# Optimization experiments

Measured on AMD Instinct MI355X. Metric: run time of the kernel, lower is better.

## Reference

```python
import jax, jax.numpy as jnp
import numpy as np

D_EEG = 256; D_QUERY = 256; D_MODEL = 256; NUM_HEADS = 8
D_HEAD = D_MODEL // NUM_HEADS; PROJ_DIM = 40
B = 32; N = 4096


def _rope(x):
    # x: (B, S, H, D) -- rotate along sequence dim with interleaved-pair convention
    S, D = x.shape[1], x.shape[-1]
    inv = 1.0 / (10000.0 ** (jnp.arange(0, D, 2, dtype=jnp.float32) / D))
    f = jnp.arange(S, dtype=jnp.float32)[:, None] * inv[None, :]        # (S, D/2)
    cos = jnp.repeat(jnp.cos(f), 2, axis=-1)[None, :, None, :]
    sin = jnp.repeat(jnp.sin(f), 2, axis=-1)[None, :, None, :]
    xp = x.reshape(x.shape[:-1] + (D // 2, 2))
    rot = jnp.stack([-xp[..., 1], xp[..., 0]], axis=-1).reshape(x.shape)
    return x * cos + rot * sin


def _ln(x, g, b):
    m = x.mean(-1, keepdims=True)
    v = x.var(-1, keepdims=True)
    return (x - m) / jnp.sqrt(v + 1e-5) * g + b


def _l2norm(x):
    return x / jnp.maximum(jnp.linalg.norm(x, axis=-1, keepdims=True), 1e-12)


def setup_inputs():
    key = jax.random.key(0)
    ks = jax.random.split(key, 16)

    def lin(k, din, dout):
        s = 1.0 / np.sqrt(din)
        w = jax.random.uniform(k, (din, dout), minval=-s, maxval=s, dtype=jnp.float32)
        b = jax.random.uniform(jax.random.fold_in(k, 1), (dout,), minval=-s, maxval=s, dtype=jnp.float32)
        return w, b

    eeg_w, eeg_b = lin(ks[0], D_EEG, D_MODEL)
    stim_w, stim_b = lin(ks[1], D_QUERY, D_MODEL)
    temp_w, temp_b = lin(ks[2], D_QUERY, D_MODEL)
    q_w, q_b = lin(ks[3], D_MODEL, D_MODEL)
    k_w, k_b = lin(ks[4], D_MODEL, D_MODEL)
    v_w, v_b = lin(ks[5], D_MODEL, D_MODEL)
    fc_w, fc_b = lin(ks[6], D_MODEL, PROJ_DIM)

    return {
        "eeg_feat": jax.random.normal(ks[7], (B, N, D_EEG), dtype=jnp.float32),
        "stim_feat": jax.random.normal(ks[8], (B, D_QUERY), dtype=jnp.float32),
        "temp_feat": jax.random.normal(ks[9], (B, D_QUERY), dtype=jnp.float32),
        "eeg_w": eeg_w, "eeg_b": eeg_b,
        "stim_w": stim_w, "stim_b": stim_b,
        "temp_w": temp_w, "temp_b": temp_b,
        "q_w": q_w, "q_b": q_b,
        "k_w": k_w, "k_b": k_b,
        "v_w": v_w, "v_b": v_b,
        "fc_w": fc_w, "fc_b": fc_b,
        "lnq_g": jnp.ones((D_MODEL,), jnp.float32), "lnq_b": jnp.zeros((D_MODEL,), jnp.float32),
        "lnk_g": jnp.ones((D_MODEL,), jnp.float32), "lnk_b": jnp.zeros((D_MODEL,), jnp.float32),
    }


def reference(eeg_feat, stim_feat, temp_feat, eeg_w, eeg_b, stim_w, stim_b,
              temp_w, temp_b, q_w, q_b, k_w, k_b, v_w, v_b, fc_w, fc_b,
              lnq_g, lnq_b, lnk_g, lnk_b):
    Bq = eeg_feat.shape[0]
    eeg = eeg_feat @ eeg_w + eeg_b                      # (B, N, D)
    stim = (stim_feat @ stim_w + stim_b)[:, None, :]
    temp = (temp_feat @ temp_w + temp_b)[:, None, :]
    query = jnp.concatenate([stim, temp], axis=1)        # (B, 2, D)

    query = _ln(query, lnq_g, lnq_b)
    kv = _ln(eeg, lnk_g, lnk_b)

    Q = (query @ q_w + q_b).reshape(Bq, 2, NUM_HEADS, D_HEAD)
    K = (kv @ k_w + k_b).reshape(Bq, -1, NUM_HEADS, D_HEAD)
    V = (kv @ v_w + v_b).reshape(Bq, -1, NUM_HEADS, D_HEAD)

    Q = _l2norm(_rope(Q))
    K = _l2norm(_rope(K))

    scores = jnp.einsum('bqhd,bkhd->bhqk', Q, K) / np.sqrt(D_HEAD)
    scale = jax.lax.stop_gradient(
        jnp.maximum(jnp.std(scores, axis=-1, ddof=1, keepdims=True), 1e-3))
    scores = jnp.tanh(scores / (2.0 * scale)) * (5.0 * scale)

    w = jax.nn.softmax(scores, axis=-1)
    w = (w + 1e-4) / (w.sum(-1, keepdims=True) + 1e-8)

    attn_out = jnp.einsum('bhqk,bkhd->bqhd', w, V).reshape(Bq, 2, D_MODEL)
    pooled = attn_out.mean(axis=1)
    logits = pooled @ fc_w + fc_b
    return logits, pooled, attn_out, query
```

## Files before the change

### kernel.cpp

```cpp
#include <hip/hip_runtime.h>
#include <hip/hip_bf16.h>
#include <math.h>

#define TID ((int)threadIdx.x)

typedef float f32x4 __attribute__((ext_vector_type(4)));
typedef short s16x8 __attribute__((ext_vector_type(8)));

__device__ __forceinline__ unsigned short f2bf(float f) {
  union { float f; unsigned u; } v; v.f = f;
  unsigned r = v.u + 0x7FFFu + ((v.u >> 16) & 1u);
  return (unsigned short)(r >> 16);
}
__device__ __forceinline__ float bf2f(unsigned short h) {
  union { unsigned u; float f; } v; v.u = ((unsigned)h) << 16;
  return v.f;
}

__global__ __launch_bounds__(256) void prep1_kernel(
    const float* __restrict__ We, const float* __restrict__ Wk,
    const float* __restrict__ g, const float* __restrict__ be,
    const float* __restrict__ bln, const float* __restrict__ kb,
    unsigned short* __restrict__ wf, float2* __restrict__ trig,
    float* __restrict__ ckv, float* __restrict__ gkv, float* __restrict__ bkv) {
  int blk = blockIdx.x;
  if (blk < 32) {
    int fi = blk * 256 + TID;
    int l = fi & 63, ks = (fi >> 6) & 7, cbG = fi >> 9;
    int col = cbG * 16 + (l & 15);
    int kbase = ks * 32 + ((l >> 4) & 3) * 8;
    s16x8 pk;
#pragma unroll
    for (int e = 0; e < 8; ++e) pk[e] = (short)f2bf(We[(size_t)(kbase + e) * 256 + col]);
    *(s16x8*)&wf[(size_t)fi * 8] = pk;
  } else if (blk < 288) {
    int e = (blk - 32) * 256 + TID;
    int n = e >> 4, p = e & 15;
    float inv = exp2f(-(float)p * 0.8304820237218406f);
    float a = (float)n * inv;
    trig[e] = make_float2(cosf(a), sinf(a));
  } else {
    int j = TID;
    float a1 = 0.f, a2 = 0.f, a3 = 0.f;
    for (int k = 0; k < 256; ++k) {
      float wkj = Wk[k * 256 + j];
      float gk = g[k];
      a1 = fmaf(be[k] * gk, wkj, a1);
      a2 = fmaf(gk, wkj, a2);
      a3 = fmaf(bln[k], wkj, a3);
    }
    ckv[j] = a1; gkv[j] = a2; bkv[j] = a3 + kb[j];
  }
}

__global__ __launch_bounds__(256) void prep2_kernel(
    const float* __restrict__ We, const float* __restrict__ Wk,
    const float* __restrict__ g, unsigned short* __restrict__ wf) {
  int j = blockIdx.x;
  __shared__ float a[256];
  __shared__ float WeC[256 * 33];
  a[TID] = g[TID] * Wk[TID * 256 + j];
  float acc = 0.f;
  for (int k0 = 0; k0 < 256; k0 += 32) {
    __syncthreads();
    const float4* src = (const float4*)&We[TID * 256 + k0];
#pragma unroll
    for (int q4 = 0; q4 < 8; ++q4) {
      float4 v = src[q4];
      WeC[TID * 33 + q4 * 4 + 0] = v.x;
      WeC[TID * 33 + q4 * 4 + 1] = v.y;
      WeC[TID * 33 + q4 * 4 + 2] = v.z;
      WeC[TID * 33 + q4 * 4 + 3] = v.w;
    }
    __syncthreads();
#pragma unroll
    for (int kk = 0; kk < 32; ++kk)
      acc = fmaf(WeC[TID * 33 + kk], a[k0 + kk], acc);
  }
  int cbG = 16 + (j >> 4), c = j & 15;
  int ks = TID >> 5, g3 = (TID >> 3) & 3, e = TID & 7;
  size_t pos = (((size_t)(cbG * 8 + ks) * 64) + g3 * 16 + c) * 8 + e;
  wf[pos] = f2bf(acc);
}

__global__ __launch_bounds__(256) void q_kernel(
    const float* __restrict__ stim_feat, const float* __restrict__ temp_feat,
    const float* __restrict__ stim_w, const float* __restrict__ stim_b,
    const float* __restrict__ temp_w, const float* __restrict__ temp_b,
    const float* __restrict__ q_w, const float* __restrict__ q_b,
    const float* __restrict__ lnq_g, const float* __restrict__ lnq_b,
    float* __restrict__ out_query, float* __restrict__ qhat) {
  int b = blockIdx.x >> 1, q = blockIdx.x & 1;
  __shared__ float f[256];
  __shared__ float red[8];
  const float* feat = (q ? temp_feat : stim_feat) + b * 256;
  const float* W = q ? temp_w : stim_w;
  const float* bias = q ? temp_b : stim_b;
  f[TID] = feat[TID];
  __syncthreads();
  float acc = bias[TID];
#pragma unroll 8
  for (int i = 0; i < 256; ++i) acc = fmaf(f[i], W[i * 256 + TID], acc);
  float s1 = acc, s2 = acc * acc;
#pragma unroll
  for (int m = 1; m < 64; m <<= 1) { s1 += __shfl_xor(s1, m, 64); s2 += __shfl_xor(s2, m, 64); }
  if ((TID & 63) == 0) { red[TID >> 6] = s1; red[4 + (TID >> 6)] = s2; }
  __syncthreads();
  s1 = red[0] + red[1] + red[2] + red[3];
  s2 = red[4] + red[5] + red[6] + red[7];
  float mean = s1 * (1.f / 256.f);
  float var = s2 * (1.f / 256.f) - mean * mean;
  float rstd = rsqrtf(var + 1e-5f);
  float qln = (acc - mean) * rstd * lnq_g[TID] + lnq_b[TID];
  out_query[(b * 2 + q) * 256 + TID] = qln;
  __syncthreads();
  f[TID] = qln;
  __syncthreads();
  float a2 = q_b[TID];
#pragma unroll 8
  for (int i = 0; i < 256; ++i) a2 = fmaf(f[i], q_w[i * 256 + TID], a2);
  __syncthreads();
  f[TID] = a2;
  __syncthreads();
  float partner = f[TID ^ 1];
  int p = (TID >> 1) & 15;
  float inv = exp2f(-(float)p * 0.8304820237218406f);
  float ang = (float)q * inv;
  float cc_ = cosf(ang), ss_ = sinf(ang);
  float r = (TID & 1) ? fmaf(a2, cc_, partner * ss_) : fmaf(a2, cc_, -partner * ss_);
  float sq = r * r;
#pragma unroll
  for (int m = 1; m < 32; m <<= 1) sq += __shfl_xor(sq, m, 32);
  float rs = 1.f / fmaxf(sqrtf(sq), 1e-12f);
  qhat[(b * 2 + q) * 256 + TID] = r * rs;
}

__global__ __launch_bounds__(256) void main2_kernel(
    const float* __restrict__ x,
    const float* __restrict__ eeg_b,
    const unsigned short* __restrict__ wf,
    const float2* __restrict__ trig,
    const float* __restrict__ qhat,
    const float* __restrict__ ckv,
    const float* __restrict__ gkv,
    const float* __restrict__ bkv,
    float2* __restrict__ stats,
    float* __restrict__ scores) {

  __shared__ __align__(16) unsigned short A[32 * 256];
  __shared__ float CV0[256];
  __shared__ float CV1[256];
  __shared__ float CV2[256];
  __shared__ float QH[512];
  __shared__ float PS[32 * 9];
  __shared__ float2 ST[32];

  const int tid = TID;
  const int w = tid >> 6, l = tid & 63, g = l >> 4, c = l & 15;
  const int r0 = blockIdx.x * 32;
  const int b = r0 >> 12;
  const int n0 = r0 & 4095;

#pragma unroll
  for (int i = 0; i < 4; ++i) {
    int ch = i * 256 + tid;
    int row = ch >> 5, cc = ch & 31;
    const float4* gp = (const float4*)(x + (size_t)(r0 + row) * 256 + cc * 8);
    float4 u0 = gp[0], u1 = gp[1];
    s16x8 pk;
    pk[0] = (short)f2bf(u0.x); pk[1] = (short)f2bf(u0.y);
    pk[2] = (short)f2bf(u0.z); pk[3] = (short)f2bf(u0.w);
    pk[4] = (short)f2bf(u1.x); pk[5] = (short)f2bf(u1.y);
    pk[6] = (short)f2bf(u1.z); pk[7] = (short)f2bf(u1.w);
    *(s16x8*)&A[row * 256 + ((cc ^ (row & 7)) * 8)] = pk;
  }
  CV0[tid] = ckv[tid]; CV1[tid] = gkv[tid]; CV2[tid] = bkv[tid];
  QH[tid] = qhat[(size_t)b * 512 + tid];
  QH[256 + tid] = qhat[(size_t)b * 512 + 256 + tid];
  __syncthreads();

  f32x4 acc[2][8];
#pragma unroll
  for (int rb = 0; rb < 2; ++rb)
#pragma unroll
    for (int cb = 0; cb < 8; ++cb) acc[rb][cb] = (f32x4){0.f, 0.f, 0.f, 0.f};
#pragma unroll
  for (int ks = 0; ks < 8; ++ks) {
    s16x8 af[2];
#pragma unroll
    for (int rb = 0; rb < 2; ++rb) {
      int row = rb * 16 + c; int kc = ks * 4 + g;
      af[rb] = *(const s16x8*)&A[row * 256 + ((kc ^ (row & 7)) * 8)];
    }
#pragma unroll
    for (int hb = 0; hb < 2; ++hb) {
      s16x8 bf4[4];
#pragma unroll
      for (int q4 = 0; q4 < 4; ++q4) {
        int cbG = w * 8 + hb * 4 + q4;
        bf4[q4] = *(const s16x8*)&wf[(size_t)((cbG * 8 + ks) * 64 + l) * 8];
      }
#pragma unroll
      for (int rb = 0; rb < 2; ++rb)
#pragma unroll
        for (int q4 = 0; q4 < 4; ++q4)
          acc[rb][hb * 4 + q4] = __builtin_amdgcn_mfma_f32_16x16x32_bf16(
              af[rb], bf4[q4], acc[rb][hb * 4 + q4], 0, 0, 0);
    }
  }

  if (w < 2) {
    float ebias[8];
#pragma unroll
    for (int cb = 0; cb < 8; ++cb) ebias[cb] = eeg_b[w * 128 + cb * 16 + c];
    float ps[2][4], pq[2][4];
#pragma unroll
    for (int rb = 0; rb < 2; ++rb)
#pragma unroll
      for (int r = 0; r < 4; ++r) {
        float s = 0.f, q2 = 0.f;
#pragma unroll
        for (int cb = 0; cb < 8; ++cb) {
          float v = acc[rb][cb][r] + ebias[cb];
          s += v; q2 += v * v;
        }
        ps[rb][r] = s; pq[rb][r] = q2;
      }
#pragma unroll
    for (int m = 1; m < 16; m <<= 1)
#pragma unroll
      for (int rb = 0; rb < 2; ++rb)
#pragma unroll
        for (int r = 0; r < 4; ++r) {
          ps[rb][r] += __shfl_xor(ps[rb][r], m, 64);
          pq[rb][r] += __shfl_xor(pq[rb][r], m, 64);
        }
    float outS = 0.f, outQ = 0.f;
#pragma unroll
    for (int rb = 0; rb < 2; ++rb)
#pragma unroll
      for (int r = 0; r < 4; ++r)
        if (c == rb * 4 + r) { outS = ps[rb][r]; outQ = pq[rb][r]; }
    if (c < 8) {
      int row = (c >> 2) * 16 + g * 4 + (c & 3);
      PS[row * 9 + w * 2 + 0] = outS;
      PS[row * 9 + w * 2 + 1] = outQ;
    }
  }
  __syncthreads();

  if (tid < 32) {
    float s = PS[tid * 9 + 0] + PS[tid * 9 + 2];
    float q2 = PS[tid * 9 + 1] + PS[tid * 9 + 3];
    float mean = s * (1.f / 256.f);
    float var = q2 * (1.f / 256.f) - mean * mean;
    float rstd = rsqrtf(var + 1e-5f);
    ST[tid] = make_float2(mean, rstd);
    stats[(size_t)r0 + tid] = make_float2(mean, rstd);
  }
  if (w >= 2) {
#pragma unroll
    for (int rb = 0; rb < 2; ++rb)
#pragma unroll
      for (int r = 0; r < 4; ++r) {
        int row = rb * 16 + g * 4 + r;
#pragma unroll
        for (int cb = 0; cb < 8; ++cb) {
          int kcol = (w - 2) * 128 + cb * 16 + c;
          A[row * 256 + (kcol ^ ((row & 7) * 8))] = f2bf(acc[rb][cb][r]);
        }
      }
  }
  __syncthreads();

  {
    int h = tid >> 5, row = tid & 31;
    float2 st = ST[row];
    float is = st.y, mis = st.x * st.y;
    const float2* tgp = trig + (size_t)(n0 + row) * 16;
    float ssq = 0.f, d0 = 0.f, d1 = 0.f;
#pragma unroll
    for (int j = 0; j < 4; ++j) {
      int u = h * 4 + j;
      s16x8 kvv = *(const s16x8*)&A[row * 256 + ((u ^ (row & 7)) * 8)];
      float2 t0 = tgp[j * 4 + 0], t1 = tgp[j * 4 + 1], t2 = tgp[j * 4 + 2], t3 = tgp[j * 4 + 3];
      float2 tg4[4] = {t0, t1, t2, t3};
#pragma unroll
      for (int t = 0; t < 4; ++t) {
        int col = h * 32 + j * 8 + 2 * t;
        float base0 = fmaf(CV0[col], is, fmaf(-mis, CV1[col], CV2[col]));
        float base1 = fmaf(CV0[col + 1], is, fmaf(-mis, CV1[col + 1], CV2[col + 1]));
        float k0 = fmaf(bf2f((unsigned short)kvv[2 * t]), is, base0);
        float k1 = fmaf(bf2f((unsigned short)kvv[2 * t + 1]), is, base1);
        float2 cs = tg4[t];
        float rv0 = k0 * cs.x - k1 * cs.y;
        float rv1 = fmaf(k1, cs.x, k0 * cs.y);
        ssq = fmaf(rv0, rv0, fmaf(rv1, rv1, ssq));
        d0 = fmaf(rv0, QH[col], fmaf(rv1, QH[col + 1], d0));
        d1 = fmaf(rv0, QH[256 + col], fmaf(rv1, QH[256 + col + 1], d1));
      }
    }
    float isv = 0.17677669529663687f / fmaxf(sqrtf(ssq), 1e-12f);
    scores[(size_t)((b * 8 + h) * 2 + 0) * 4096 + n0 + row] = d0 * isv;
    scores[(size_t)((b * 8 + h) * 2 + 1) * 4096 + n0 + row] = d1 * isv;
  }
}

__global__ __launch_bounds__(256) void wgt_kernel(
    const float* __restrict__ scores, const float2* __restrict__ stats,
    float* __restrict__ wbuf, float2* __restrict__ sbuf) {
  int b = blockIdx.x >> 3, h = blockIdx.x & 7;
  const float* s0p = scores + (size_t)((b * 8 + h) * 2 + 0) * 4096;
  const float* s1p = scores + (size_t)((b * 8 + h) * 2 + 1) * 4096;
  float sa[16], sb[16];
  float a1 = 0.f, a2 = 0.f, b1 = 0.f, b2 = 0.f;
#pragma unroll
  for (int i = 0; i < 16; ++i) {
    int k = i * 256 + TID;
    sa[i] = s0p[k]; sb[i] = s1p[k];
    a1 += sa[i]; a2 += sa[i] * sa[i];
    b1 += sb[i]; b2 += sb[i] * sb[i];
  }
  __shared__ float red[16];
  int w = TID >> 6;
#pragma unroll
  for (int m = 1; m < 64; m <<= 1) {
    a1 += __shfl_xor(a1, m, 64); a2 += __shfl_xor(a2, m, 64);
    b1 += __shfl_xor(b1, m, 64); b2 += __shfl_xor(b2, m, 64);
  }
  if ((TID & 63) == 0) { red[w * 4] = a1; red[w * 4 + 1] = a2; red[w * 4 + 2] = b1; red[w * 4 + 3] = b2; }
  __syncthreads();
  a1 = red[0] + red[4] + red[8] + red[12];
  a2 = red[1] + red[5] + red[9] + red[13];
  b1 = red[2] + red[6] + red[10] + red[14];
  b2 = red[3] + red[7] + red[11] + red[15];
  float va = (a2 - a1 * a1 * (1.f / 4096.f)) * (1.f / 4095.f);
  float vb = (b2 - b1 * b1 * (1.f / 4096.f)) * (1.f / 4095.f);
  float sga = fmaxf(sqrtf(fmaxf(va, 0.f)), 1e-3f);
  float sgb = fmaxf(sqrtf(fmaxf(vb, 0.f)), 1e-3f);
  float ia = 0.5f / sga, ib = 0.5f / sgb;
  float fa = 5.f * sga, fb = 5.f * sgb;
  float ea = 0.f, eb = 0.f;
#pragma unroll
  for (int i = 0; i < 16; ++i) {
    sa[i] = __expf(tanhf(sa[i] * ia) * fa);
    sb[i] = __expf(tanhf(sb[i] * ib) * fb);
    ea += sa[i]; eb += sb[i];
  }
#pragma unroll
  for (int m = 1; m < 64; m <<= 1) { ea += __shfl_xor(ea, m, 64); eb += __shfl_xor(eb, m, 64); }
  __syncthreads();
  if ((TID & 63) == 0) { red[w * 2] = ea; red[w * 2 + 1] = eb; }
  __syncthreads();
  ea = red[0] + red[2] + red[4] + red[6];
  eb = red[1] + red[3] + red[5] + red[7];
  float iea = 1.f / ea, ieb = 1.f / eb;
  float* w0 = wbuf + ((size_t)(b * 16) + h * 2 + 0) * 4096;
  float* w1 = w0 + 4096;
  float s1a = 0.f, s2a = 0.f, s1b = 0.f, s2b = 0.f;
#pragma unroll
  for (int i = 0; i < 16; ++i) {
    int k = i * 256 + TID;
    float2 st = stats[(size_t)b * 4096 + k];
    float wa = fmaf(sa[i], iea, 1e-4f);
    float wb = fmaf(sb[i], ieb, 1e-4f);
    float wta = wa * st.y, wtb = wb * st.y;
    w0[k] = wta; w1[k] = wtb;
    s1a += wta; s2a = fmaf(wta, st.x, s2a);
    s1b += wtb; s2b = fmaf(wtb, st.x, s2b);
  }
#pragma unroll
  for (int m = 1; m < 64; m <<= 1) {
    s1a += __shfl_xor(s1a, m, 64); s2a += __shfl_xor(s2a, m, 64);
    s1b += __shfl_xor(s1b, m, 64); s2b += __shfl_xor(s2b, m, 64);
  }
  __syncthreads();
  if ((TID & 63) == 0) { red[w * 4] = s1a; red[w * 4 + 1] = s2a; red[w * 4 + 2] = s1b; red[w * 4 + 3] = s2b; }
  __syncthreads();
  if (TID == 0) {
    sbuf[((size_t)(b * 8 + h)) * 2 + 0] =
        make_float2(red[0] + red[4] + red[8] + red[12], red[1] + red[5] + red[9] + red[13]);
    sbuf[((size_t)(b * 8 + h)) * 2 + 1] =
        make_float2(red[2] + red[6] + red[10] + red[14], red[3] + red[7] + red[11] + red[15]);
  }
}

__global__ __launch_bounds__(256) void ysum_kernel(
    const float* __restrict__ x, const float* __restrict__ wbuf,
    float* __restrict__ ypart) {
  int b = blockIdx.x >> 5, slab = blockIdx.x & 31;
  int h = TID >> 5, cg = TID & 31;
  const float* xb = x + ((size_t)(b * 4096 + slab * 128)) * 256 + cg * 8;
  const float* w0 = wbuf + ((size_t)(b * 16) + h * 2 + 0) * 4096 + slab * 128;
  const float* w1 = w0 + 4096;
  float y0[8], y1[8];
#pragma unroll
  for (int t = 0; t < 8; ++t) { y0[t] = 0.f; y1[t] = 0.f; }
#pragma unroll 4
  for (int r = 0; r < 128; ++r) {
    const float4* fp = (const float4*)(xb + (size_t)r * 256);
    float4 va = fp[0], vb4 = fp[1];
    float wa = w0[r], wc = w1[r];
    y0[0] = fmaf(wa, va.x, y0[0]);  y1[0] = fmaf(wc, va.x, y1[0]);
    y0[1] = fmaf(wa, va.y, y0[1]);  y1[1] = fmaf(wc, va.y, y1[1]);
    y0[2] = fmaf(wa, va.z, y0[2]);  y1[2] = fmaf(wc, va.z, y1[2]);
    y0[3] = fmaf(wa, va.w, y0[3]);  y1[3] = fmaf(wc, va.w, y1[3]);
    y0[4] = fmaf(wa, vb4.x, y0[4]); y1[4] = fmaf(wc, vb4.x, y1[4]);
    y0[5] = fmaf(wa, vb4.y, y0[5]); y1[5] = fmaf(wc, vb4.y, y1[5]);
    y0[6] = fmaf(wa, vb4.z, y0[6]); y1[6] = fmaf(wc, vb4.z, y1[6]);
    y0[7] = fmaf(wa, vb4.w, y0[7]); y1[7] = fmaf(wc, vb4.w, y1[7]);
  }
  float* yp = ypart + (((size_t)(b * 32 + slab) * 16) + h * 2) * 256 + cg * 8;
  *(float4*)&yp[0] = (float4){y0[0], y0[1], y0[2], y0[3]};
  *(float4*)&yp[4] = (float4){y0[4], y0[5], y0[6], y0[7]};
  *(float4*)&yp[256] = (float4){y1[0], y1[1], y1[2], y1[3]};
  *(float4*)&yp[260] = (float4){y1[4], y1[5], y1[6], y1[7]};
}

__global__ __launch_bounds__(256) void yz_kernel(
    const float* __restrict__ ypart, const float2* __restrict__ sbuf,
    const float* __restrict__ We, const float* __restrict__ be,
    const float* __restrict__ g, const float* __restrict__ bln,
    float* __restrict__ zbuf) {
  int b = blockIdx.x >> 4, hq = blockIdx.x & 15;
  __shared__ float Y[256];
  float s = 0.f;
#pragma unroll 8
  for (int sl = 0; sl < 32; ++sl)
    s += ypart[(((size_t)(b * 32 + sl) * 16) + hq) * 256 + TID];
  Y[TID] = s;
  __syncthreads();
  float2 s12 = sbuf[(size_t)b * 16 + hq];
  int k = TID;
  float t = s12.x * be[k];
#pragma unroll 8
  for (int cc = 0; cc < 256; ++cc)
    t = fmaf(Y[cc], We[cc * 256 + k], t);
  zbuf[((size_t)(b * 16) + hq) * 256 + k] = (t - s12.y) * g[k] + 1.4096f * bln[k];
}

__global__ __launch_bounds__(256) void att_kernel(
    const float* __restrict__ zbuf, const float* __restrict__ v_w,
    const float* __restrict__ v_b, float* __restrict__ out_attn,
    float* __restrict__ out_pooled) {
  int b = blockIdx.x >> 3, h = blockIdx.x & 7;
  __shared__ float ZA[2][256];
  __shared__ float ATTs[2][32];
  {
    int q = TID >> 7, cc = TID & 127;
    const float* zp = zbuf + ((size_t)(b * 16) + h * 2 + q) * 256;
    ZA[q][cc] = zp[cc];
    ZA[q][128 + cc] = zp[128 + cc];
  }
  __syncthreads();
  int q = TID >> 7, dl = (TID >> 2) & 31, quarter = TID & 3;
  int dout = h * 32 + dl;
  float ps = 0.f;
#pragma unroll 8
  for (int i = 0; i < 64; ++i) {
    int cc = quarter * 64 + i;
    ps = fmaf(ZA[q][cc], v_w[cc * 256 + dout], ps);
  }
  ps += __shfl_xor(ps, 1, 64);
  ps += __shfl_xor(ps, 2, 64);
  if (quarter == 0) {
    float val = ps + 1.4096f * v_b[dout];
    out_attn[(b * 2 + q) * 256 + dout] = val;
    ATTs[q][dl] = val;
  }
  __syncthreads();
  if (TID < 32) {
    out_pooled[b * 256 + h * 32 + TID] = 0.5f * (ATTs[0][TID] + ATTs[1][TID]);
  }
}

__global__ __launch_bounds__(256) void logit_kernel(
    const float* __restrict__ out_pooled, const float* __restrict__ fc_w,
    const float* __restrict__ fc_b, float* __restrict__ out_logits) {
  int b = blockIdx.x;
  __shared__ float P[256];
  P[TID] = out_pooled[b * 256 + TID];
  __syncthreads();
  if (TID < 40) {
    float acc = fc_b[TID];
#pragma unroll 8
    for (int i = 0; i < 256; ++i) acc = fmaf(P[i], fc_w[i * 40 + TID], acc);
    out_logits[b * 40 + TID] = acc;
  }
}

extern "C" void kernel_launch(void* const* d_in, const int* in_sizes, int n_in,
                              void* d_out, int out_size, void* d_ws, size_t ws_size,
                              hipStream_t stream) {
  (void)in_sizes; (void)n_in; (void)out_size; (void)ws_size;
  const float* eeg_feat  = (const float*)d_in[0];
  const float* stim_feat = (const float*)d_in[1];
  const float* temp_feat = (const float*)d_in[2];
  const float* eeg_w = (const float*)d_in[3];
  const float* eeg_b = (const float*)d_in[4];
  const float* stim_w = (const float*)d_in[5];
  const float* stim_b = (const float*)d_in[6];
  const float* temp_w = (const float*)d_in[7];
  const float* temp_b = (const float*)d_in[8];
  const float* q_w = (const float*)d_in[9];
  const float* q_b = (const float*)d_in[10];
  const float* k_w = (const float*)d_in[11];
  const float* k_b = (const float*)d_in[12];
  const float* v_w = (const float*)d_in[13];
  const float* v_b = (const float*)d_in[14];
  const float* fc_w = (const float*)d_in[15];
  const float* fc_b = (const float*)d_in[16];
  const float* lnq_g = (const float*)d_in[17];
  const float* lnq_b = (const float*)d_in[18];
  const float* lnk_g = (const float*)d_in[19];
  const float* lnk_b = (const float*)d_in[20];

  char* ws = (char*)d_ws;
  unsigned short* wfr = (unsigned short*)(ws + 0);
  float2* trig        = (float2*)(ws + 262144);
  float* qhat         = (float*)(ws + 786432);
  float* ckv          = (float*)(ws + 851968);
  float* gkv          = (float*)(ws + 852992);
  float* bkv          = (float*)(ws + 854016);
  float2* sbuf        = (float2*)(ws + 855040);
  float2* stats       = (float2*)(ws + 1048576);
  float* scores       = (float*)(ws + 2097152);
  float* wbuf         = (float*)(ws + 10485760);
  float* ypart        = (float*)(ws + 18874368);
  float* zbuf         = (float*)(ws + 35651584);

  float* out = (float*)d_out;
  float* out_logits = out;
  float* out_pooled = out + 1280;
  float* out_attn   = out + 9472;
  float* out_query  = out + 25856;

  prep1_kernel<<<289, 256, 0, stream>>>(eeg_w, k_w, lnk_g, eeg_b, lnk_b, k_b,
                                        wfr, trig, ckv, gkv, bkv);
  prep2_kernel<<<256, 256, 0, stream>>>(eeg_w, k_w, lnk_g, wfr);
  q_kernel<<<64, 256, 0, stream>>>(stim_feat, temp_feat, stim_w, stim_b,
                                   temp_w, temp_b, q_w, q_b, lnq_g, lnq_b,
                                   out_query, qhat);
  main2_kernel<<<4096, 256, 0, stream>>>(eeg_feat, eeg_b, wfr, trig, qhat,
                                         ckv, gkv, bkv, stats, scores);
  wgt_kernel<<<256, 256, 0, stream>>>(scores, stats, wbuf, sbuf);
  ysum_kernel<<<1024, 256, 0, stream>>>(eeg_feat, wbuf, ypart);
  yz_kernel<<<512, 256, 0, stream>>>(ypart, sbuf, eeg_w, eeg_b, lnk_g, lnk_b, zbuf);
  att_kernel<<<256, 256, 0, stream>>>(zbuf, v_w, v_b, out_attn, out_pooled);
  logit_kernel<<<32, 256, 0, stream>>>(out_pooled, fc_w, fc_b, out_logits);
}
```

Before: 216.8 us.

## Process four row tiles per block with register-prefetched next tile

The main scoring kernel now has each block handle 128 rows as four 32-row tiles, launching 1024 blocks instead of 4096. While the current tile's MFMA and epilogue run, the next tile's fp32 input and RoPE trig values are prefetched into registers. Trig values are staged in shared memory rather than read per thread from global. This is meant to hide global load latency behind compute and amortise per-block setup (qhat, LN constants), at the cost of more registers, extra barriers and fewer blocks for occupancy.

```diff
diff --git a/kernel.cpp b/kernel.cpp
--- a/kernel.cpp
+++ b/kernel.cpp
@@ -154,155 +154,190 @@
   __shared__ float QH[512];
   __shared__ float PS[32 * 9];
   __shared__ float2 ST[32];
+  __shared__ float COS[32][17];
+  __shared__ float SIN[32][17];
 
   const int tid = TID;
   const int w = tid >> 6, l = tid & 63, g = l >> 4, c = l & 15;
-  const int r0 = blockIdx.x * 32;
-  const int b = r0 >> 12;
-  const int n0 = r0 & 4095;
-
-#pragma unroll
-  for (int i = 0; i < 4; ++i) {
-    int ch = i * 256 + tid;
-    int row = ch >> 5, cc = ch & 31;
-    const float4* gp = (const float4*)(x + (size_t)(r0 + row) * 256 + cc * 8);
-    float4 u0 = gp[0], u1 = gp[1];
-    s16x8 pk;
-    pk[0] = (short)f2bf(u0.x); pk[1] = (short)f2bf(u0.y);
-    pk[2] = (short)f2bf(u0.z); pk[3] = (short)f2bf(u0.w);
-    pk[4] = (short)f2bf(u1.x); pk[5] = (short)f2bf(u1.y);
-    pk[6] = (short)f2bf(u1.z); pk[7] = (short)f2bf(u1.w);
-    *(s16x8*)&A[row * 256 + ((cc ^ (row & 7)) * 8)] = pk;
-  }
+  const int chunk0 = blockIdx.x * 128;
+  const int b = chunk0 >> 12;
+  const int n0b = chunk0 & 4095;
+
   CV0[tid] = ckv[tid]; CV1[tid] = gkv[tid]; CV2[tid] = bkv[tid];
   QH[tid] = qhat[(size_t)b * 512 + tid];
   QH[256 + tid] = qhat[(size_t)b * 512 + 256 + tid];
-  __syncthreads();
-
-  f32x4 acc[2][8];
-#pragma unroll
-  for (int rb = 0; rb < 2; ++rb)
-#pragma unroll
-    for (int cb = 0; cb < 8; ++cb) acc[rb][cb] = (f32x4){0.f, 0.f, 0.f, 0.f};
-#pragma unroll
-  for (int ks = 0; ks < 8; ++ks) {
-    s16x8 af[2];
-#pragma unroll
-    for (int rb = 0; rb < 2; ++rb) {
-      int row = rb * 16 + c; int kc = ks * 4 + g;
-      af[rb] = *(const s16x8*)&A[row * 256 + ((kc ^ (row & 7)) * 8)];
-    }
-#pragma unroll
-    for (int hb = 0; hb < 2; ++hb) {
-      s16x8 bf4[4];
-#pragma unroll
-      for (int q4 = 0; q4 < 4; ++q4) {
-        int cbG = w * 8 + hb * 4 + q4;
-        bf4[q4] = *(const s16x8*)&wf[(size_t)((cbG * 8 + ks) * 64 + l) * 8];
+
+  float4 sxa[4], sxb[4];
+  float2 tf0, tf1;
+  {
+    const float* xt = x + (size_t)chunk0 * 256;
+#pragma unroll
+    for (int i = 0; i < 4; ++i) {
+      int ch = i * 256 + tid, row = ch >> 5, cc = ch & 31;
+      const float4* gp = (const float4*)(xt + row * 256 + cc * 8);
+      sxa[i] = gp[0]; sxb[i] = gp[1];
+    }
+    tf0 = trig[(size_t)(n0b + (tid >> 4)) * 16 + (tid & 15)];
+    tf1 = trig[(size_t)(n0b + 16 + (tid >> 4)) * 16 + (tid & 15)];
+  }
+
+  for (int t = 0; t < 4; ++t) {
+    const int r0 = chunk0 + t * 32;
+    const int n0 = n0b + t * 32;
+
+    if (t) __syncthreads();
+#pragma unroll
+    for (int i = 0; i < 4; ++i) {
+      int ch = i * 256 + tid, row = ch >> 5, cc = ch & 31;
+      s16x8 pk;
+      pk[0] = (short)f2bf(sxa[i].x); pk[1] = (short)f2bf(sxa[i].y);
+      pk[2] = (short)f2bf(sxa[i].z); pk[3] = (short)f2bf(sxa[i].w);
+      pk[4] = (short)f2bf(sxb[i].x); pk[5] = (short)f2bf(sxb[i].y);
+      pk[6] = (short)f2bf(sxb[i].z); pk[7] = (short)f2bf(sxb[i].w);
+      *(s16x8*)&A[row * 256 + ((cc ^ (row & 7)) * 8)] = pk;
+    }
+    {
+      int row = tid >> 4, p = tid & 15;
+      COS[row][p] = tf0.x; SIN[row][p] = tf0.y;
+      COS[16 + row][p] = tf1.x; SIN[16 + row][p] = tf1.y;
+    }
+    __syncthreads();
+
+    if (t < 3) {
+      const float* xt = x + (size_t)(r0 + 32) * 256;
+#pragma unroll
+      for (int i = 0; i < 4; ++i) {
+        int ch = i * 256 + tid, row = ch >> 5, cc = ch & 31;
+        const float4* gp = (const float4*)(xt + row * 256 + cc * 8);
+        sxa[i] = gp[0]; sxb[i] = gp[1];
       }
+      tf0 = trig[(size_t)(n0 + 32 + (tid >> 4)) * 16 + (tid & 15)];
+      tf1 = trig[(size_t)(n0 + 48 + (tid >> 4)) * 16 + (tid & 15)];
+    }
+
+    f32x4 acc[2][8];
+#pragma unroll
+    for (int rb = 0; rb < 2; ++rb)
+#pragma unroll
+      for (int cb = 0; cb < 8; ++cb) acc[rb][cb] = (f32x4){0.f, 0.f, 0.f, 0.f};
+#pragma unroll
+    for (int ks = 0; ks < 8; ++ks) {
+      s16x8 af[2];
+#pragma unroll
+      for (int rb = 0; rb < 2; ++rb) {
+        int row = rb * 16 + c; int kc = ks * 4 + g;
+        af[rb] = *(const s16x8*)&A[row * 256 + ((kc ^ (row & 7)) * 8)];
+      }
+#pragma unroll
+      for (int hb = 0; hb < 2; ++hb) {
+        s16x8 bf4[4];
+#pragma unroll
+        for (int q4 = 0; q4 < 4; ++q4) {
+          int cbG = w * 8 + hb * 4 + q4;
+          bf4[q4] = *(const s16x8*)&wf[(size_t)((cbG * 8 + ks) * 64 + l) * 8];
+        }
+#pragma unroll
+        for (int rb = 0; rb < 2; ++rb)
+#pragma unroll
+          for (int q4 = 0; q4 < 4; ++q4)
+            acc[rb][hb * 4 + q4] = __builtin_amdgcn_mfma_f32_16x16x32_bf16(
+                af[rb], bf4[q4], acc[rb][hb * 4 + q4], 0, 0, 0);
+      }
+    }
+
+    if (w < 2) {
+      float ebias[8];
+#pragma unroll
+      for (int cb = 0; cb < 8; ++cb) ebias[cb] = eeg_b[w * 128 + cb * 16 + c];
+      float ps[2][4], pq[2][4];
 #pragma unroll
       for (int rb = 0; rb < 2; ++rb)
 #pragma unroll
-        for (int q4 = 0; q4 < 4; ++q4)
-          acc[rb][hb * 4 + q4] = __builtin_amdgcn_mfma_f32_16x16x32_bf16(
-              af[rb], bf4[q4], acc[rb][hb * 4 + q4], 0, 0, 0);
-    }
-  }
-
-  if (w < 2) {
-    float ebias[8];
-#pragma unroll
-    for (int cb = 0; cb < 8; ++cb) ebias[cb] = eeg_b[w * 128 + cb * 16 + c];
-    float ps[2][4], pq[2][4];
-#pragma unroll
-    for (int rb = 0; rb < 2; ++rb)
-#pragma unroll
-      for (int r = 0; r < 4; ++r) {
-        float s = 0.f, q2 = 0.f;
-#pragma unroll
-        for (int cb = 0; cb < 8; ++cb) {
-          float v = acc[rb][cb][r] + ebias[cb];
-          s += v; q2 += v * v;
+        for (int r = 0; r < 4; ++r) {
+          float s = 0.f, q2 = 0.f;
+#pragma unroll
+          for (int cb = 0; cb < 8; ++cb) {
+            float v = acc[rb][cb][r] + ebias[cb];
+            s += v; q2 += v * v;
+          }
+          ps[rb][r] = s; pq[rb][r] = q2;
         }
-        ps[rb][r] = s; pq[rb][r] = q2;
+#pragma unroll
+      for (int m = 1; m < 16; m <<= 1)
+#pragma unroll
+        for (int rb = 0; rb < 2; ++rb)
+#pragma unroll
+          for (int r = 0; r < 4; ++r) {
+            ps[rb][r] += __shfl_xor(ps[rb][r], m, 64);
+            pq[rb][r] += __shfl_xor(pq[rb][r], m, 64);
+          }
+      float outS = 0.f, outQ = 0.f;
+#pragma unroll
+      for (int rb = 0; rb < 2; ++rb)
+#pragma unroll
+        for (int r = 0; r < 4; ++r)
+          if (c == rb * 4 + r) { outS = ps[rb][r]; outQ = pq[rb][r]; }
+      if (c < 8) {
+        int row = (c >> 2) * 16 + g * 4 + (c & 3);
+        PS[row * 9 + w * 2 + 0] = outS;
+        PS[row * 9 + w * 2 + 1] = outQ;
       }
-#pragma unroll
-    for (int m = 1; m < 16; m <<= 1)
+    }
+    __syncthreads();
+
+    if (tid < 32) {
+      float s = PS[tid * 9 + 0] + PS[tid * 9 + 2];
+      float q2 = PS[tid * 9 + 1] + PS[tid * 9 + 3];
+      float mean = s * (1.f / 256.f);
+      float var = q2 * (1.f / 256.f) - mean * mean;
+      float rstd = rsqrtf(var + 1e-5f);
+      ST[tid] = make_float2(mean, rstd);
+      stats[(size_t)r0 + tid] = make_float2(mean, rstd);
+    }
+    if (w >= 2) {
 #pragma unroll
       for (int rb = 0; rb < 2; ++rb)
 #pragma unroll
         for (int r = 0; r < 4; ++r) {
-          ps[rb][r] += __shfl_xor(ps[rb][r], m, 64);
-          pq[rb][r] += __shfl_xor(pq[rb][r], m, 64);
+          int row = rb * 16 + g * 4 + r;
+#pragma unroll
+          for (int cb = 0; cb < 8; ++cb) {
+            int kcol = (w - 2) * 128 + cb * 16 + c;
+            A[row * 256 + (kcol ^ ((row & 7) * 8))] = f2bf(acc[rb][cb][r]);
+          }
         }
-    float outS = 0.f, outQ = 0.f;
-#pragma unroll
-    for (int rb = 0; rb < 2; ++rb)
-#pragma unroll
-      for (int r = 0; r < 4; ++r)
-        if (c == rb * 4 + r) { outS = ps[rb][r]; outQ = pq[rb][r]; }
-    if (c < 8) {
-      int row = (c >> 2) * 16 + g * 4 + (c & 3);
-      PS[row * 9 + w * 2 + 0] = outS;
-      PS[row * 9 + w * 2 + 1] = outQ;
-    }
-  }
-  __syncthreads();
-
-  if (tid < 32) {
-    float s = PS[tid * 9 + 0] + PS[tid * 9 + 2];
-    float q2 = PS[tid * 9 + 1] + PS[tid * 9 + 3];
-    float mean = s * (1.f / 256.f);
-    float var = q2 * (1.f / 256.f) - mean * mean;
-    float rstd = rsqrtf(var + 1e-5f);
-    ST[tid] = make_float2(mean, rstd);
-    stats[(size_t)r0 + tid] = make_float2(mean, rstd);
-  }
-  if (w >= 2) {
-#pragma unroll
-    for (int rb = 0; rb < 2; ++rb)
-#pragma unroll
-      for (int r = 0; r < 4; ++r) {
-        int row = rb * 16 + g * 4 + r;
-#pragma unroll
-        for (int cb = 0; cb < 8; ++cb) {
-          int kcol = (w - 2) * 128 + cb * 16 + c;
-          A[row * 256 + (kcol ^ ((row & 7) * 8))] = f2bf(acc[rb][cb][r]);
+    }
+    __syncthreads();
+
+    {
+      int h = tid >> 5, row = tid & 31;
+      float2 st = ST[row];
+      float is = st.y, mis = st.x * st.y;
+      float ssq = 0.f, d0 = 0.f, d1 = 0.f;
+#pragma unroll
+      for (int j = 0; j < 4; ++j) {
+        int u = h * 4 + j;
+        s16x8 kvv = *(const s16x8*)&A[row * 256 + ((u ^ (row & 7)) * 8)];
+#pragma unroll
+        for (int t4 = 0; t4 < 4; ++t4) {
+          int col = h * 32 + j * 8 + 2 * t4;
+          int pp = j * 4 + t4;
+          float base0 = fmaf(CV0[col], is, fmaf(-mis, CV1[col], CV2[col]));
+          float base1 = fmaf(CV0[col + 1], is, fmaf(-mis, CV1[col + 1], CV2[col + 1]));
+          float k0 = fmaf(bf2f((unsigned short)kvv[2 * t4]), is, base0);
+          float k1 = fmaf(bf2f((unsigned short)kvv[2 * t4 + 1]), is, base1);
+          float cx = COS[row][pp], sx = SIN[row][pp];
+          float rv0 = k0 * cx - k1 * sx;
+          float rv1 = fmaf(k1, cx, k0 * sx);
+          ssq = fmaf(rv0, rv0, fmaf(rv1, rv1, ssq));
+          d0 = fmaf(rv0, QH[col], fmaf(rv1, QH[col + 1], d0));
+          d1 = fmaf(rv0, QH[256 + col], fmaf(rv1, QH[256 + col + 1], d1));
         }
       }
-  }
-  __syncthreads();
-
-  {
-    int h = tid >> 5, row = tid & 31;
-    float2 st = ST[row];
-    float is = st.y, mis = st.x * st.y;
-    const float2* tgp = trig + (size_t)(n0 + row) * 16;
-    float ssq = 0.f, d0 = 0.f, d1 = 0.f;
-#pragma unroll
-    for (int j = 0; j < 4; ++j) {
-      int u = h * 4 + j;
-      s16x8 kvv = *(const s16x8*)&A[row * 256 + ((u ^ (row & 7)) * 8)];
-      float2 t0 = tgp[j * 4 + 0], t1 = tgp[j * 4 + 1], t2 = tgp[j * 4 + 2], t3 = tgp[j * 4 + 3];
-      float2 tg4[4] = {t0, t1, t2, t3};
-#pragma unroll
-      for (int t = 0; t < 4; ++t) {
-        int col = h * 32 + j * 8 + 2 * t;
-        float base0 = fmaf(CV0[col], is, fmaf(-mis, CV1[col], CV2[col]));
-        float base1 = fmaf(CV0[col + 1], is, fmaf(-mis, CV1[col + 1], CV2[col + 1]));
-        float k0 = fmaf(bf2f((unsigned short)kvv[2 * t]), is, base0);
-        float k1 = fmaf(bf2f((unsigned short)kvv[2 * t + 1]), is, base1);
-        float2 cs = tg4[t];
-        float rv0 = k0 * cs.x - k1 * cs.y;
-        float rv1 = fmaf(k1, cs.x, k0 * cs.y);
-        ssq = fmaf(rv0, rv0, fmaf(rv1, rv1, ssq));
-        d0 = fmaf(rv0, QH[col], fmaf(rv1, QH[col + 1], d0));
-        d1 = fmaf(rv0, QH[256 + col], fmaf(rv1, QH[256 + col + 1], d1));
-      }
-    }
-    float isv = 0.17677669529663687f / fmaxf(sqrtf(ssq), 1e-12f);
-    scores[(size_t)((b * 8 + h) * 2 + 0) * 4096 + n0 + row] = d0 * isv;
-    scores[(size_t)((b * 8 + h) * 2 + 1) * 4096 + n0 + row] = d1 * isv;
+      float isv = 0.17677669529663687f / fmaxf(sqrtf(ssq), 1e-12f);
+      scores[(size_t)((b * 8 + h) * 2 + 0) * 4096 + n0 + row] = d0 * isv;
+      scores[(size_t)((b * 8 + h) * 2 + 1) * 4096 + n0 + row] = d1 * isv;
+    }
   }
 }
 
@@ -541,7 +576,7 @@
   q_kernel<<<64, 256, 0, stream>>>(stim_feat, temp_feat, stim_w, stim_b,
                                    temp_w, temp_b, q_w, q_b, lnq_g, lnq_b,
                                    out_query, qhat);
-  main2_kernel<<<4096, 256, 0, stream>>>(eeg_feat, eeg_b, wfr, trig, qhat,
+  main2_kernel<<<1024, 256, 0, stream>>>(eeg_feat, eeg_b, wfr, trig, qhat,
                                          ckv, gkv, bkv, stats, scores);
   wgt_kernel<<<256, 256, 0, stream>>>(scores, stats, wbuf, sbuf);
   ysum_kernel<<<1024, 256, 0, stream>>>(eeg_feat, wbuf, ypart);
```

New measurement: 396.8 us. +83.1%, slower.
